# Kernel tuning notes

Hardware: AMD Instinct MI355X
Metric: run time of the kernel (lower is better)

## Reference

```python
import jax, jax.numpy as jnp
import numpy as np

NUM_GRAPHS = 64

def _sage(x, edge_index, Wl, bl, Wr):
    # PyG SAGEConv (mean aggr): out = lin_l(mean_{j in N(i)} x_j) + lin_r(x_i)
    src, dst = edge_index[0], edge_index[1]
    n = x.shape[0]
    summed = jax.ops.segment_sum(x[src], dst, num_segments=n)        # [N,F]
    deg = jax.ops.segment_sum(jnp.ones_like(src, dtype=x.dtype), dst, num_segments=n)
    agg = summed / jnp.maximum(deg, 1.0)[:, None]
    return agg @ Wl.T + bl + x @ Wr.T

def setup_inputs() -> dict:
    key = jax.random.key(0)
    ks = jax.random.split(key, 12)
    N, E, F, H = 50000, 600000, 128, 128
    x = jax.random.normal(ks[0], (N, F), dtype=jnp.float32)
    edge_index = jax.random.randint(ks[1], (2, E), 0, N, dtype=jnp.int64)
    batch = jnp.sort(jax.random.randint(ks[2], (N,), 0, NUM_GRAPHS, dtype=jnp.int64))
    s = lambda fan_in: 1.0 / np.sqrt(fan_in)
    return {
        "x": x, "edge_index": edge_index, "batch": batch,
        "W1l": jax.random.uniform(ks[3], (H, F), minval=-s(F), maxval=s(F)),
        "b1l": jnp.zeros((H,), jnp.float32),
        "W1r": jax.random.uniform(ks[4], (H, F), minval=-s(F), maxval=s(F)),
        "W2l": jax.random.uniform(ks[5], (H, H), minval=-s(H), maxval=s(H)),
        "b2l": jnp.zeros((H,), jnp.float32),
        "W2r": jax.random.uniform(ks[6], (H, H), minval=-s(H), maxval=s(H)),
        "Wc1": jax.random.uniform(ks[7], (H, H), minval=-s(H), maxval=s(H)),
        "bc1": jax.random.uniform(ks[8], (H,), minval=-s(H), maxval=s(H)),
        "Wc2": jax.random.uniform(ks[9], (1, H), minval=-s(H), maxval=s(H)),
        "bc2": jax.random.uniform(ks[10], (1,), minval=-s(H), maxval=s(H)),
    }

def reference(x, edge_index, batch, W1l, b1l, W1r, W2l, b2l, W2r, Wc1, bc1, Wc2, bc2):
    h = jax.nn.relu(_sage(x, edge_index, W1l, b1l, W1r))
    h = jax.nn.relu(_sage(h, edge_index, W2l, b2l, W2r))
    # global mean pool per graph
    gsum = jax.ops.segment_sum(h, batch, num_segments=NUM_GRAPHS)
    gcnt = jax.ops.segment_sum(jnp.ones((h.shape[0],), h.dtype), batch, num_segments=NUM_GRAPHS)
    gemb = gsum / jnp.maximum(gcnt, 1.0)[:, None]                    # [G,H]
    # classifier MLP (dropout = identity in eval)
    z = jax.nn.relu(gemb @ Wc1.T + bc1)
    out = (z @ Wc2.T + bc2).squeeze(-1)                              # [G]
    return out
```

## Files before the change

kernel.cpp:

```cpp
#include <hip/hip_runtime.h>


typedef __attribute__((ext_vector_type(8))) short bf16x8;
typedef __attribute__((ext_vector_type(8))) unsigned short ushort8;
typedef __attribute__((ext_vector_type(4))) float f32x4;

#define HBLK 4096

__device__ inline unsigned short f2bf(float f) {
  unsigned u = __float_as_uint(f);
  u += 0x7fff + ((u >> 16) & 1);
  return (unsigned short)(u >> 16);
}
__device__ inline float bf2f(unsigned short h) { return __uint_as_float(((unsigned)h) << 16); }


__device__ inline void wprep_body(int id, const float* __restrict__ Wl, const float* __restrict__ Wr,
                                  unsigned short* __restrict__ Bpre) {
  if (id >= 4096) return;
  int kk = id >> 9;
  int ct = (id >> 6) & 7;
  int l  = id & 63;
  int colIdx = ct * 16 + (l & 15);
  int k0 = kk * 32 + (l >> 4) * 8;
  const float* W = (k0 < 128) ? Wl : Wr;
  int kb = k0 & 127;
#pragma unroll
  for (int j = 0; j < 8; ++j) {
    float v = W[colIdx * 128 + kb + j];
    unsigned short h = f2bf(v);
    size_t bh = (size_t)kk * 8192 + ((size_t)ct * 64 + l) * 8 + j;
    Bpre[bh] = h;
    Bpre[bh + 4096] = f2bf(v - bf2f(h));
  }
}

__global__ __launch_bounds__(256) void k_prep(
    const float* __restrict__ x, unsigned short* __restrict__ xbf, int total,
    const float* __restrict__ W1l, const float* __restrict__ W1r, unsigned short* __restrict__ Bpre1,
    const float* __restrict__ W2l, const float* __restrict__ W2r, unsigned short* __restrict__ Bpre2,
    const int* __restrict__ batch, int* __restrict__ gcnt, float* __restrict__ gsum, int N,
    const int* __restrict__ ei, int* __restrict__ bhist, int E,
    int nTobf, int nEblk) {
  __shared__ int h[256];
  int b = blockIdx.x;
  int tid = threadIdx.x;
  if (b < nTobf) {
    int i = (b * 256 + tid) * 4;
    if (i + 3 < total) {
      float4 v = *(const float4*)(x + i);
      ushort4 p;
      p.x = f2bf(v.x); p.y = f2bf(v.y); p.z = f2bf(v.z); p.w = f2bf(v.w);
      *(ushort4*)(xbf + i) = p;
    } else {
      for (int k = 0; k < 4 && i + k < total; ++k) xbf[i + k] = f2bf(x[i + k]);
    }
  } else if (b < nTobf + 16) {
    wprep_body((b - nTobf) * 256 + tid, W1l, W1r, Bpre1);
  } else if (b < nTobf + 32) {
    wprep_body((b - nTobf - 16) * 256 + tid, W2l, W2r, Bpre2);
  } else if (b < nTobf + 32 + nEblk) {
    int eb = b - nTobf - 32;
    h[tid] = 0;
    __syncthreads();
    int base = eb * HBLK;
    int end = min(base + HBLK, E);
    for (int e = base + tid; e < end; e += 256) atomicAdd(&h[ei[E + e] >> 8], 1);
    __syncthreads();
    bhist[eb * 256 + tid] = h[tid];
  } else {
    for (int i = tid; i < 64 * 128; i += 256) gsum[i] = 0.f;
    if (tid < 64) {
      int g = tid;
      int lo = 0, hi = N;
      while (lo < hi) { int mid = (lo + hi) >> 1; if (batch[mid] < g) lo = mid + 1; else hi = mid; }
      int a = lo;
      lo = 0; hi = N;
      while (lo < hi) { int mid = (lo + hi) >> 1; if (batch[mid] < g + 1) lo = mid + 1; else hi = mid; }
      gcnt[g] = lo - a;
    }
  }
}


__global__ __launch_bounds__(256) void k_bscan_a(const int* __restrict__ bhist, int* __restrict__ bukbase,
                                                 int nblk) {
  __shared__ int s[256];
  int t = threadIdx.x;
  int sum = 0;
  for (int b = 0; b < nblk; ++b) sum += bhist[b * 256 + t];
  s[t] = sum;
  __syncthreads();
  for (int d = 1; d < 256; d <<= 1) {
    int v = (t >= d) ? s[t - d] : 0;
    __syncthreads();
    s[t] += v;
    __syncthreads();
  }
  bukbase[t] = s[t] - sum;
  if (t == 255) bukbase[256] = s[255];
}

__global__ __launch_bounds__(256) void k_bscan_b(int* __restrict__ bhist, const int* __restrict__ bukbase,
                                                 int nblk) {
  __shared__ int s[256];
  int buk = blockIdx.x;
  int t = threadIdx.x;
  int c = (t < nblk) ? bhist[t * 256 + buk] : 0;
  s[t] = c;
  __syncthreads();
  for (int d = 1; d < 256; d <<= 1) {
    int v = (t >= d) ? s[t - d] : 0;
    __syncthreads();
    s[t] += v;
    __syncthreads();
  }
  if (t < nblk) bhist[t * 256 + buk] = bukbase[buk] + s[t] - c;
}

__global__ __launch_bounds__(256) void k_scat(const int* __restrict__ ei, const int* __restrict__ bhist,
                                              unsigned* __restrict__ ebuk, int E) {
  __shared__ int cur[256];
  int tid = threadIdx.x;
  cur[tid] = bhist[blockIdx.x * 256 + tid];
  __syncthreads();
  int base = blockIdx.x * HBLK;
  int end = min(base + HBLK, E);
  for (int e = base + tid; e < end; e += 256) {
    int d = ei[E + e];
    int srcv = ei[e];
    int p = atomicAdd(&cur[d >> 8], 1);
    ebuk[p] = ((unsigned)(d & 255) << 24) | (unsigned)srcv;
  }
}

__global__ __launch_bounds__(256) void k_bucket(const unsigned* __restrict__ ebuk,
                                                const int* __restrict__ bukbase,
                                                int* __restrict__ off, int* __restrict__ colv,
                                                int N, int E) {
  __shared__ int h[256];
  __shared__ int cur[256];
  __shared__ int sc[256];
  int tid = threadIdx.x;
  int buk = blockIdx.x;
  int b0 = bukbase[buk], b1 = bukbase[buk + 1];
  h[tid] = 0;
  __syncthreads();
  for (int i = b0 + tid; i < b1; i += 256) atomicAdd(&h[ebuk[i] >> 24], 1);
  __syncthreads();
  int my = h[tid];
  sc[tid] = my;
  __syncthreads();
  for (int d = 1; d < 256; d <<= 1) {
    int v = (tid >= d) ? sc[tid - d] : 0;
    __syncthreads();
    sc[tid] += v;
    __syncthreads();
  }
  int excl = sc[tid] - my;
  cur[tid] = excl;
  int node = buk * 256 + tid;
  if (node < N) off[node] = b0 + excl;
  if (buk == gridDim.x - 1 && tid == 0) off[N] = E;
  __syncthreads();
  for (int i = b0 + tid; i < b1; i += 256) {
    unsigned v = ebuk[i];
    int p = atomicAdd(&cur[v >> 24], 1);
    colv[b0 + p] = (int)(v & 0xFFFFFFu);
  }
}


__global__ __launch_bounds__(256) void k_agg_bf(const unsigned short* __restrict__ Xbf,
                                                const int* __restrict__ off, const int* __restrict__ col,
                                                unsigned short* __restrict__ Tbf, int N) {
  int wid = (blockIdx.x * 256 + threadIdx.x) >> 6;
  int ln = threadIdx.x & 63;
  if (wid >= N) return;
  int o0 = off[wid], o1 = off[wid + 1];
  int deg = o1 - o0;
  int rs = ln >> 4, fs = ln & 15;
  float acc[8];
#pragma unroll
  for (int j = 0; j < 8; ++j) acc[j] = 0.f;

  for (int base = 0; base < deg; base += 16) {
#pragma unroll
    for (int u = 0; u < 4; ++u) {
      int n = base + u * 4 + rs;
      if (n < deg) {
        int idx = col[o0 + n];
        ushort8 q = *(const ushort8*)(Xbf + (size_t)idx * 128 + fs * 8);
#pragma unroll
        for (int j = 0; j < 8; ++j) acc[j] += bf2f(q[j]);
      }
    }
  }
#pragma unroll
  for (int j = 0; j < 8; ++j) {
    acc[j] += __shfl_xor(acc[j], 16);
    acc[j] += __shfl_xor(acc[j], 32);
  }
  if (rs == 0) {
    float sc = 1.0f / (float)max(deg, 1);
    unsigned short w[8];
#pragma unroll
    for (int j = 0; j < 8; ++j) w[j] = f2bf(acc[j] * sc);
    uint4 uw;
    uw.x = (unsigned)w[0] | ((unsigned)w[1] << 16);
    uw.y = (unsigned)w[2] | ((unsigned)w[3] << 16);
    uw.z = (unsigned)w[4] | ((unsigned)w[5] << 16);
    uw.w = (unsigned)w[6] | ((unsigned)w[7] << 16);
    *(uint4*)(Tbf + (size_t)wid * 128 + fs * 8) = uw;
  }
}


__global__ __launch_bounds__(256) void k_lin_mfma(
    const unsigned short* __restrict__ Tbf,
    const float* __restrict__ Xf,
    const unsigned short* __restrict__ Xbf,
    const unsigned short* __restrict__ Bpre,
    const float* __restrict__ bias,
    unsigned short* __restrict__ OUTbf,
    const int* __restrict__ batch, float* __restrict__ gsum,
    int N, int mode) {
  __shared__ unsigned short As[4096];
  __shared__ unsigned short Bs[8192];
  __shared__ float ps[128];

  int tid = threadIdx.x;
  int wv = tid >> 6, ln = tid & 63;
  int rowBase = blockIdx.x * 64;

  int sRow = tid >> 2;
  int sKq = tid & 3;
  int sgr = min(rowBase + sRow, N - 1);
  int sSlot = ((sRow >> 4) * 64 + (sKq << 4) + (sRow & 15)) * 8;

  f32x4 acc[4][2];
#pragma unroll
  for (int rg = 0; rg < 4; ++rg) {
    acc[rg][0] = (f32x4){0.f, 0.f, 0.f, 0.f};
    acc[rg][1] = (f32x4){0.f, 0.f, 0.f, 0.f};
  }

  const uint4* BpreV = (const uint4*)Bpre;

  for (int kk = 0; kk < 8; ++kk) {
    bool selfTerm = (kk >= 4);
    int kOff = (kk & 3) * 32 + sKq * 8;
    uint4 b0 = BpreV[kk * 1024 + tid];
    uint4 b1 = BpreV[kk * 1024 + tid + 256];
    uint4 b2 = BpreV[kk * 1024 + tid + 512];
    uint4 b3 = BpreV[kk * 1024 + tid + 768];

    uint4 uh = {0u, 0u, 0u, 0u}, ul = {0u, 0u, 0u, 0u};
    bool doLo = selfTerm && (mode == 0);
    if (!selfTerm) {
      uh = *(const uint4*)(Tbf + (size_t)sgr * 128 + kOff);
    } else if (mode == 1) {
      uh = *(const uint4*)(Xbf + (size_t)sgr * 128 + kOff);
    } else {
      float4 p0 = *(const float4*)(Xf + (size_t)sgr * 128 + kOff);
      float4 p1 = *(const float4*)(Xf + (size_t)sgr * 128 + kOff + 4);
      float fv[8] = {p0.x, p0.y, p0.z, p0.w, p1.x, p1.y, p1.z, p1.w};
      unsigned short hh[8], ll[8];
#pragma unroll
      for (int j = 0; j < 8; ++j) {
        unsigned short h = f2bf(fv[j]);
        hh[j] = h;
        ll[j] = f2bf(fv[j] - bf2f(h));
      }
      uh.x = (unsigned)hh[0] | ((unsigned)hh[1] << 16);
      uh.y = (unsigned)hh[2] | ((unsigned)hh[3] << 16);
      uh.z = (unsigned)hh[4] | ((unsigned)hh[5] << 16);
      uh.w = (unsigned)hh[6] | ((unsigned)hh[7] << 16);
      ul.x = (unsigned)ll[0] | ((unsigned)ll[1] << 16);
      ul.y = (unsigned)ll[2] | ((unsigned)ll[3] << 16);
      ul.z = (unsigned)ll[4] | ((unsigned)ll[5] << 16);
      ul.w = (unsigned)ll[6] | ((unsigned)ll[7] << 16);
    }

    __syncthreads();
    *(uint4*)(As + sSlot) = uh;
    if (doLo) *(uint4*)(As + 2048 + sSlot) = ul;
    uint4* BsV = (uint4*)Bs;
    BsV[tid] = b0;
    BsV[tid + 256] = b1;
    BsV[tid + 512] = b2;
    BsV[tid + 768] = b3;
    __syncthreads();

    int c0 = wv * 2;
    bf16x8 bh0 = *(bf16x8*)(Bs + ((size_t)c0 * 64 + ln) * 8);
    bf16x8 bl0 = *(bf16x8*)(Bs + 4096 + ((size_t)c0 * 64 + ln) * 8);
    bf16x8 bh1 = *(bf16x8*)(Bs + ((size_t)(c0 + 1) * 64 + ln) * 8);
    bf16x8 bl1 = *(bf16x8*)(Bs + 4096 + ((size_t)(c0 + 1) * 64 + ln) * 8);
#pragma unroll
    for (int rg = 0; rg < 4; ++rg) {
      bf16x8 ah = *(bf16x8*)(As + ((size_t)rg * 64 + ln) * 8);
      acc[rg][0] = __builtin_amdgcn_mfma_f32_16x16x32_bf16(ah, bh0, acc[rg][0], 0, 0, 0);
      acc[rg][0] = __builtin_amdgcn_mfma_f32_16x16x32_bf16(ah, bl0, acc[rg][0], 0, 0, 0);
      acc[rg][1] = __builtin_amdgcn_mfma_f32_16x16x32_bf16(ah, bh1, acc[rg][1], 0, 0, 0);
      acc[rg][1] = __builtin_amdgcn_mfma_f32_16x16x32_bf16(ah, bl1, acc[rg][1], 0, 0, 0);
      if (doLo) {
        bf16x8 al = *(bf16x8*)(As + 2048 + ((size_t)rg * 64 + ln) * 8);
        acc[rg][0] = __builtin_amdgcn_mfma_f32_16x16x32_bf16(al, bh0, acc[rg][0], 0, 0, 0);
        acc[rg][1] = __builtin_amdgcn_mfma_f32_16x16x32_bf16(al, bh1, acc[rg][1], 0, 0, 0);
      }
    }
  }

  int lcol = ln & 15;
  int rsub = (ln >> 4) * 4;
#pragma unroll
  for (int c = 0; c < 2; ++c) {
    float b = bias[(wv * 2 + c) * 16 + lcol];
#pragma unroll
    for (int rg = 0; rg < 4; ++rg)
#pragma unroll
      for (int r = 0; r < 4; ++r) acc[rg][c][r] = fmaxf(acc[rg][c][r] + b, 0.f);
  }

  if (mode == 0) {
#pragma unroll
    for (int rg = 0; rg < 4; ++rg)
#pragma unroll
      for (int r = 0; r < 4; ++r) {
        int row = rowBase + rg * 16 + rsub + r;
        if (row < N) {
          OUTbf[(size_t)row * 128 + (wv * 2 + 0) * 16 + lcol] = f2bf(acc[rg][0][r]);
          OUTbf[(size_t)row * 128 + (wv * 2 + 1) * 16 + lcol] = f2bf(acc[rg][1][r]);
        }
      }
  } else {
    if (tid < 128) ps[tid] = 0.f;
    __syncthreads();
    int lastRow = min(rowBase + 63, N - 1);
    int g0 = batch[rowBase], g1 = batch[lastRow];
    if (g0 == g1) {
#pragma unroll
      for (int c = 0; c < 2; ++c) {
        float s = 0.f;
#pragma unroll
        for (int rg = 0; rg < 4; ++rg)
#pragma unroll
          for (int r = 0; r < 4; ++r) {
            int row = rowBase + rg * 16 + rsub + r;
            if (row < N) s += acc[rg][c][r];
          }
        atomicAdd(&ps[(wv * 2 + c) * 16 + lcol], s);
      }
      __syncthreads();
      if (tid < 128) atomicAdd(&gsum[g0 * 128 + tid], ps[tid]);
    } else {
#pragma unroll
      for (int rg = 0; rg < 4; ++rg)
#pragma unroll
        for (int r = 0; r < 4; ++r) {
          int row = rowBase + rg * 16 + rsub + r;
          if (row < N) {
            int g = batch[row];
            atomicAdd(&gsum[g * 128 + (wv * 2 + 0) * 16 + lcol], acc[rg][0][r]);
            atomicAdd(&gsum[g * 128 + (wv * 2 + 1) * 16 + lcol], acc[rg][1][r]);
          }
        }
    }
  }
}


__global__ __launch_bounds__(128) void k_cls(const float* __restrict__ gsum, const int* __restrict__ gcnt,
                                             const float* __restrict__ Wc1, const float* __restrict__ bc1,
                                             const float* __restrict__ Wc2, const float* __restrict__ bc2,
                                             float* __restrict__ out) {
  __shared__ float red[128];
  int g = blockIdx.x;
  int h = threadIdx.x;
  float inv = 1.0f / (float)max(gcnt[g], 1);
  float s = 0.f;
  for (int f = 0; f < 128; ++f) s += gsum[g * 128 + f] * Wc1[h * 128 + f];
  red[h] = fmaxf(s * inv + bc1[h], 0.f) * Wc2[h];
  __syncthreads();
  for (int d = 64; d > 0; d >>= 1) {
    if (h < d) red[h] += red[h + d];
    __syncthreads();
  }
  if (h == 0) out[g] = red[0] + bc2[0];
}


extern "C" void kernel_launch(void* const* d_in, const int* in_sizes, int n_in,
                              void* d_out, int out_size, void* d_ws, size_t ws_size,
                              hipStream_t stream) {
  const float* x   = (const float*)d_in[0];
  const int*   ei  = (const int*)d_in[1];
  const int*   bat = (const int*)d_in[2];
  const float* W1l = (const float*)d_in[3];
  const float* b1l = (const float*)d_in[4];
  const float* W1r = (const float*)d_in[5];
  const float* W2l = (const float*)d_in[6];
  const float* b2l = (const float*)d_in[7];
  const float* W2r = (const float*)d_in[8];
  const float* Wc1 = (const float*)d_in[9];
  const float* bc1 = (const float*)d_in[10];
  const float* Wc2 = (const float*)d_in[11];
  const float* bc2 = (const float*)d_in[12];
  float* out = (float*)d_out;

  int N = in_sizes[0] / 128;
  int E = in_sizes[1] / 2;
  int nEblk = (E + HBLK - 1) / HBLK;
  int nBuk = (N + 255) >> 8;
  int total = N * 128;
  int nTobf = (total / 4 + 255) / 256;

  char* ws = (char*)d_ws;
  size_t o = 0;
  auto alloc = [&](size_t bytes) {
    char* p = ws + o;
    o += (bytes + 255) & ~(size_t)255;
    return p;
  };
  int*      off    = (int*)alloc((size_t)(N + 1) * 4);
  int*      col    = (int*)alloc((size_t)E * 4);
  unsigned* ebuk   = (unsigned*)alloc((size_t)E * 4);
  int*      bhist  = (int*)alloc((size_t)nEblk * 256 * 4);
  int*      bukbase= (int*)alloc(257 * 4);
  unsigned short* Tbf  = (unsigned short*)alloc((size_t)N * 128 * 2);
  unsigned short* xbf  = (unsigned short*)alloc((size_t)N * 128 * 2);
  unsigned short* h1bf = (unsigned short*)alloc((size_t)N * 128 * 2);
  unsigned short* Bpre1 = (unsigned short*)alloc(65536 * 2);
  unsigned short* Bpre2 = (unsigned short*)alloc(65536 * 2);
  float*    gsum   = (float*)alloc(64 * 128 * 4 + 64 * 4);
  int*      gcnt   = (int*)(gsum + 64 * 128);

  k_prep<<<nTobf + 32 + nEblk + 1, 256, 0, stream>>>(
      x, xbf, total, W1l, W1r, Bpre1, W2l, W2r, Bpre2,
      bat, gcnt, gsum, N, ei, bhist, E, nTobf, nEblk);

  k_bscan_a<<<1, 256, 0, stream>>>(bhist, bukbase, nEblk);
  k_bscan_b<<<256, 256, 0, stream>>>(bhist, bukbase, nEblk);
  k_scat<<<nEblk, 256, 0, stream>>>(ei, bhist, ebuk, E);
  k_bucket<<<nBuk, 256, 0, stream>>>(ebuk, bukbase, off, col, N, E);

  int nLinBlk = (N + 63) / 64;
  k_agg_bf<<<(N + 3) / 4, 256, 0, stream>>>(xbf, off, col, Tbf, N);
  k_lin_mfma<<<nLinBlk, 256, 0, stream>>>(Tbf, x, nullptr, Bpre1, b1l, h1bf, bat, gsum, N, 0);
  k_agg_bf<<<(N + 3) / 4, 256, 0, stream>>>(h1bf, off, col, Tbf, N);
  k_lin_mfma<<<nLinBlk, 256, 0, stream>>>(Tbf, nullptr, h1bf, Bpre2, b2l, nullptr, bat, gsum, N, 1);

  k_cls<<<64, 128, 0, stream>>>(gsum, gcnt, Wc1, bc1, Wc2, bc2, out);
}
```

Baseline: 168.5 us.

## Load MFMA operands directly from global, drop LDS staging and fp32 self split

The linear kernel no longer stages A and B tiles through shared memory with two barriers per k-step. Each lane now loads its MFMA fragments straight from global memory (B from the prepacked weights, A from bf16 rows). The first layer's self term now reads the bf16 copy of x instead of splitting fp32 x into hi/lo parts, which removes the extra MFMAs at some cost in precision. Separately, the two bucket-scan kernels are merged into one launch in which every block recomputes the global prefix, saving a launch at the cost of redundant reads.

```diff
diff --git a/kernel.cpp b/kernel.cpp
--- a/kernel.cpp
+++ b/kernel.cpp
@@ -83,9 +83,10 @@
 }
 
 
-__global__ __launch_bounds__(256) void k_bscan_a(const int* __restrict__ bhist, int* __restrict__ bukbase,
-                                                 int nblk) {
+__global__ __launch_bounds__(256) void k_bscan(int* __restrict__ bhist, int* __restrict__ bukbase,
+                                               int nblk) {
   __shared__ int s[256];
+  int buk = blockIdx.x;
   int t = threadIdx.x;
   int sum = 0;
   for (int b = 0; b < nblk; ++b) sum += bhist[b * 256 + t];
@@ -97,15 +98,9 @@
     s[t] += v;
     __syncthreads();
   }
-  bukbase[t] = s[t] - sum;
-  if (t == 255) bukbase[256] = s[255];
-}
-
-__global__ __launch_bounds__(256) void k_bscan_b(int* __restrict__ bhist, const int* __restrict__ bukbase,
-                                                 int nblk) {
-  __shared__ int s[256];
-  int buk = blockIdx.x;
-  int t = threadIdx.x;
+  int myBase = (buk == 0) ? 0 : s[buk - 1];
+  int tot = s[255];
+  __syncthreads();
   int c = (t < nblk) ? bhist[t * 256 + buk] : 0;
   s[t] = c;
   __syncthreads();
@@ -115,7 +110,9 @@
     s[t] += v;
     __syncthreads();
   }
-  if (t < nblk) bhist[t * 256 + buk] = bukbase[buk] + s[t] - c;
+  if (t < nblk) bhist[t * 256 + buk] = myBase + s[t] - c;
+  if (t == 0) bukbase[buk] = myBase;
+  if (buk == 255 && t == 1) bukbase[256] = tot;
 }
 
 __global__ __launch_bounds__(256) void k_scat(const int* __restrict__ ei, const int* __restrict__ bhist,
@@ -216,27 +213,21 @@
 }
 
 
-__global__ __launch_bounds__(256) void k_lin_mfma(
-    const unsigned short* __restrict__ Tbf,
-    const float* __restrict__ Xf,
-    const unsigned short* __restrict__ Xbf,
+__global__ __launch_bounds__(256) void k_lin2(
+    const unsigned short* __restrict__ Agg,
+    const unsigned short* __restrict__ Self,
     const unsigned short* __restrict__ Bpre,
     const float* __restrict__ bias,
     unsigned short* __restrict__ OUTbf,
     const int* __restrict__ batch, float* __restrict__ gsum,
     int N, int mode) {
-  __shared__ unsigned short As[4096];
-  __shared__ unsigned short Bs[8192];
   __shared__ float ps[128];
-
   int tid = threadIdx.x;
   int wv = tid >> 6, ln = tid & 63;
   int rowBase = blockIdx.x * 64;
-
-  int sRow = tid >> 2;
-  int sKq = tid & 3;
-  int sgr = min(rowBase + sRow, N - 1);
-  int sSlot = ((sRow >> 4) * 64 + (sKq << 4) + (sRow & 15)) * 8;
+  int kq = (ln >> 4) * 8;
+  int rsel = ln & 15;
+  int c0 = wv * 2;
 
   f32x4 acc[4][2];
 #pragma unroll
@@ -245,70 +236,27 @@
     acc[rg][1] = (f32x4){0.f, 0.f, 0.f, 0.f};
   }
 
-  const uint4* BpreV = (const uint4*)Bpre;
-
+#pragma unroll
   for (int kk = 0; kk < 8; ++kk) {
-    bool selfTerm = (kk >= 4);
-    int kOff = (kk & 3) * 32 + sKq * 8;
-    uint4 b0 = BpreV[kk * 1024 + tid];
-    uint4 b1 = BpreV[kk * 1024 + tid + 256];
-    uint4 b2 = BpreV[kk * 1024 + tid + 512];
-    uint4 b3 = BpreV[kk * 1024 + tid + 768];
-
-    uint4 uh = {0u, 0u, 0u, 0u}, ul = {0u, 0u, 0u, 0u};
-    bool doLo = selfTerm && (mode == 0);
-    if (!selfTerm) {
-      uh = *(const uint4*)(Tbf + (size_t)sgr * 128 + kOff);
-    } else if (mode == 1) {
-      uh = *(const uint4*)(Xbf + (size_t)sgr * 128 + kOff);
-    } else {
-      float4 p0 = *(const float4*)(Xf + (size_t)sgr * 128 + kOff);
-      float4 p1 = *(const float4*)(Xf + (size_t)sgr * 128 + kOff + 4);
-      float fv[8] = {p0.x, p0.y, p0.z, p0.w, p1.x, p1.y, p1.z, p1.w};
-      unsigned short hh[8], ll[8];
-#pragma unroll
-      for (int j = 0; j < 8; ++j) {
-        unsigned short h = f2bf(fv[j]);
-        hh[j] = h;
-        ll[j] = f2bf(fv[j] - bf2f(h));
-      }
-      uh.x = (unsigned)hh[0] | ((unsigned)hh[1] << 16);
-      uh.y = (unsigned)hh[2] | ((unsigned)hh[3] << 16);
-      uh.z = (unsigned)hh[4] | ((unsigned)hh[5] << 16);
-      uh.w = (unsigned)hh[6] | ((unsigned)hh[7] << 16);
-      ul.x = (unsigned)ll[0] | ((unsigned)ll[1] << 16);
-      ul.y = (unsigned)ll[2] | ((unsigned)ll[3] << 16);
-      ul.z = (unsigned)ll[4] | ((unsigned)ll[5] << 16);
-      ul.w = (unsigned)ll[6] | ((unsigned)ll[7] << 16);
-    }
-
-    __syncthreads();
-    *(uint4*)(As + sSlot) = uh;
-    if (doLo) *(uint4*)(As + 2048 + sSlot) = ul;
-    uint4* BsV = (uint4*)Bs;
-    BsV[tid] = b0;
-    BsV[tid + 256] = b1;
-    BsV[tid + 512] = b2;
-    BsV[tid + 768] = b3;
-    __syncthreads();
-
-    int c0 = wv * 2;
-    bf16x8 bh0 = *(bf16x8*)(Bs + ((size_t)c0 * 64 + ln) * 8);
-    bf16x8 bl0 = *(bf16x8*)(Bs + 4096 + ((size_t)c0 * 64 + ln) * 8);
-    bf16x8 bh1 = *(bf16x8*)(Bs + ((size_t)(c0 + 1) * 64 + ln) * 8);
-    bf16x8 bl1 = *(bf16x8*)(Bs + 4096 + ((size_t)(c0 + 1) * 64 + ln) * 8);
+    const unsigned short* S = (kk < 4) ? Agg : Self;
+    int kOff = (kk & 3) * 32 + kq;
+    const unsigned short* Bk = Bpre + (size_t)kk * 8192;
+    bf16x8 bh0 = *(const bf16x8*)(Bk + ((size_t)c0 * 64 + ln) * 8);
+    bf16x8 bl0 = *(const bf16x8*)(Bk + 4096 + ((size_t)c0 * 64 + ln) * 8);
+    bf16x8 bh1 = *(const bf16x8*)(Bk + ((size_t)(c0 + 1) * 64 + ln) * 8);
+    bf16x8 bl1 = *(const bf16x8*)(Bk + 4096 + ((size_t)(c0 + 1) * 64 + ln) * 8);
+    bf16x8 ah[4];
 #pragma unroll
     for (int rg = 0; rg < 4; ++rg) {
-      bf16x8 ah = *(bf16x8*)(As + ((size_t)rg * 64 + ln) * 8);
-      acc[rg][0] = __builtin_amdgcn_mfma_f32_16x16x32_bf16(ah, bh0, acc[rg][0], 0, 0, 0);
-      acc[rg][0] = __builtin_amdgcn_mfma_f32_16x16x32_bf16(ah, bl0, acc[rg][0], 0, 0, 0);
-      acc[rg][1] = __builtin_amdgcn_mfma_f32_16x16x32_bf16(ah, bh1, acc[rg][1], 0, 0, 0);
-      acc[rg][1] = __builtin_amdgcn_mfma_f32_16x16x32_bf16(ah, bl1, acc[rg][1], 0, 0, 0);
-      if (doLo) {
-        bf16x8 al = *(bf16x8*)(As + 2048 + ((size_t)rg * 64 + ln) * 8);
-        acc[rg][0] = __builtin_amdgcn_mfma_f32_16x16x32_bf16(al, bh0, acc[rg][0], 0, 0, 0);
-        acc[rg][1] = __builtin_amdgcn_mfma_f32_16x16x32_bf16(al, bh1, acc[rg][1], 0, 0, 0);
-      }
+      int row = min(rowBase + rg * 16 + rsel, N - 1);
+      ah[rg] = *(const bf16x8*)(S + (size_t)row * 128 + kOff);
+    }
+#pragma unroll
+    for (int rg = 0; rg < 4; ++rg) {
+      acc[rg][0] = __builtin_amdgcn_mfma_f32_16x16x32_bf16(ah[rg], bh0, acc[rg][0], 0, 0, 0);
+      acc[rg][0] = __builtin_amdgcn_mfma_f32_16x16x32_bf16(ah[rg], bl0, acc[rg][0], 0, 0, 0);
+      acc[rg][1] = __builtin_amdgcn_mfma_f32_16x16x32_bf16(ah[rg], bh1, acc[rg][1], 0, 0, 0);
+      acc[rg][1] = __builtin_amdgcn_mfma_f32_16x16x32_bf16(ah[rg], bl1, acc[rg][1], 0, 0, 0);
     }
   }
 
@@ -440,16 +388,15 @@
       x, xbf, total, W1l, W1r, Bpre1, W2l, W2r, Bpre2,
       bat, gcnt, gsum, N, ei, bhist, E, nTobf, nEblk);
 
-  k_bscan_a<<<1, 256, 0, stream>>>(bhist, bukbase, nEblk);
-  k_bscan_b<<<256, 256, 0, stream>>>(bhist, bukbase, nEblk);
+  k_bscan<<<256, 256, 0, stream>>>(bhist, bukbase, nEblk);
   k_scat<<<nEblk, 256, 0, stream>>>(ei, bhist, ebuk, E);
   k_bucket<<<nBuk, 256, 0, stream>>>(ebuk, bukbase, off, col, N, E);
 
   int nLinBlk = (N + 63) / 64;
   k_agg_bf<<<(N + 3) / 4, 256, 0, stream>>>(xbf, off, col, Tbf, N);
-  k_lin_mfma<<<nLinBlk, 256, 0, stream>>>(Tbf, x, nullptr, Bpre1, b1l, h1bf, bat, gsum, N, 0);
+  k_lin2<<<nLinBlk, 256, 0, stream>>>(Tbf, xbf, Bpre1, b1l, h1bf, bat, gsum, N, 0);
   k_agg_bf<<<(N + 3) / 4, 256, 0, stream>>>(h1bf, off, col, Tbf, N);
-  k_lin_mfma<<<nLinBlk, 256, 0, stream>>>(Tbf, nullptr, h1bf, Bpre2, b2l, nullptr, bat, gsum, N, 1);
+  k_lin2<<<nLinBlk, 256, 0, stream>>>(Tbf, h1bf, Bpre2, b2l, nullptr, bat, gsum, N, 1);
 
   k_cls<<<64, 128, 0, stream>>>(gsum, gcnt, Wc1, bc1, Wc2, bc2, out);
 }
```

Result: slower. 181.0 us (+7.4%).
